# Kernel optimization log

Measured on AMD Instinct MI355X. Metric: run time of the kernel, lower is better.

Reference implementation:

```python
import jax, jax.numpy as jnp
import numpy as np

HEADS = 8
DIM_HEAD = 64
SCALE = DIM_HEAD ** -0.5


def setup_inputs() -> dict:
    key = jax.random.key(0)
    k1, k2, k3, k4 = jax.random.split(key, 4)
    dim = 512
    inner = HEADS * DIM_HEAD  # 512
    x = jax.random.normal(k1, (4, 2048, dim), dtype=jnp.float32)
    # torch nn.Linear weight layout: [out_features, in_features]
    w_qkv = jax.random.normal(k2, (inner * 3, dim), dtype=jnp.float32) * (dim ** -0.5)
    w_out = jax.random.normal(k3, (dim, inner), dtype=jnp.float32) * (inner ** -0.5)
    b_out = jax.random.normal(k4, (dim,), dtype=jnp.float32) * 0.01
    return {"x": x, "w_qkv": w_qkv, "w_out": w_out, "b_out": b_out}


def reference(x, w_qkv, w_out, b_out):
    b, n, _ = x.shape
    qkv = x @ w_qkv.T                                   # [b, n, 3*inner]
    q, k, v = jnp.split(qkv, 3, axis=-1)
    def to_heads(t):
        return t.reshape(b, n, HEADS, DIM_HEAD).transpose(0, 2, 1, 3)  # b h n d
    q, k, v = to_heads(q), to_heads(k), to_heads(v)
    dots = jnp.einsum('bhid,bhjd->bhij', q, k) * SCALE  # [b, h, n, n]
    attn = jax.nn.softmax(dots, axis=-1)
    out = jnp.einsum('bhij,bhjd->bhid', attn, v)        # [b, h, n, d]
    out = out.transpose(0, 2, 1, 3).reshape(b, n, HEADS * DIM_HEAD)
    return out @ w_out.T + b_out                        # [b, n, dim]
```

## Files before the change

kernel.cpp:

```cpp
#include <hip/hip_runtime.h>

typedef unsigned int u32;
typedef unsigned short u16;
typedef float f32x4 __attribute__((ext_vector_type(4)));
typedef u32 u32x4 __attribute__((ext_vector_type(4)));
typedef u32 u32x2 __attribute__((ext_vector_type(2)));

__device__ __forceinline__ u16 f2bf(float f) {
    u32 u = __builtin_bit_cast(u32, f);
    u = (u + 0x7FFFu + ((u >> 16) & 1u)) >> 16;
    return (u16)u;
}

__device__ __forceinline__ void mfma16(f32x4& d, const u32x4& a, const u32x4& b) {
    asm("v_mfma_f32_16x16x32_bf16 %0, %1, %2, %0" : "+v"(d) : "v"(a), "v"(b));
}

__device__ __forceinline__ float exp2a(float x) {
    float r;
    asm("v_exp_f32 %0, %1\n\ts_nop 1" : "=v"(r) : "v"(x));
    return r;
}
__device__ __forceinline__ u32 cvtpk(float lo, float hi) {
    u32 r;
    asm("v_cvt_pk_bf16_f32 %0, %1, %2" : "=v"(r) : "v"(lo), "v"(hi));
    return r;
}
__device__ __forceinline__ void gload_lds16(const u16* g, u16* l) {
    __builtin_amdgcn_global_load_lds(
        (const __attribute__((address_space(1))) u32*)g,
        (__attribute__((address_space(3))) u32*)l, 16, 0, 0);
}

__global__ __launch_bounds__(256) void cast2_kernel(
    const float* __restrict__ wq, const float* __restrict__ wo,
    u16* __restrict__ wqb, u16* __restrict__ wob) {
    int bid = blockIdx.x;
    const float* src;
    u16* dst;
    int base;
    if (bid < 384) { src = wq; dst = wqb; base = bid * 2048; }
    else           { src = wo; dst = wob; base = (bid - 384) * 2048; }
    int i = base + threadIdx.x * 8;
    float4 a = *(const float4*)(src + i);
    float4 b = *(const float4*)(src + i + 4);
    u32x4 r;
    r.x = (u32)f2bf(a.x) | ((u32)f2bf(a.y) << 16);
    r.y = (u32)f2bf(a.z) | ((u32)f2bf(a.w) << 16);
    r.z = (u32)f2bf(b.x) | ((u32)f2bf(b.y) << 16);
    r.w = (u32)f2bf(b.z) | ((u32)f2bf(b.w) << 16);
    *(u32x4*)(dst + i) = r;
}

__global__ __launch_bounds__(256) void gemm_qkv(
    const float* __restrict__ A32, const u16* __restrict__ B, int K,
    u16* __restrict__ qo, u16* __restrict__ ko, u16* __restrict__ vto)
{
    __shared__ __align__(16) u16 Al[128 * 64];
    __shared__ __align__(16) u16 Bl[128 * 64];
    const int t = threadIdx.x;
    const int w = t >> 6, l = t & 63;
    const int wr = w >> 1, wc = w & 1;
    const int g = l >> 4, li = l & 15;
    const int m0 = blockIdx.x * 128, n0 = blockIdx.y * 128;

    const f32x4 z = {0.f, 0.f, 0.f, 0.f};
    f32x4 acc[4][4];
#pragma unroll
    for (int mi = 0; mi < 4; ++mi)
#pragma unroll
        for (int ni = 0; ni < 4; ++ni) acc[mi][ni] = z;

    int goff[4], ldst[4];
#pragma unroll
    for (int rnd = 0; rnd < 4; ++rnd) {
        int s = rnd * 256 + t;
        int p = s >> 3, cp = s & 7;
        int cg = cp ^ (p & 7);
        goff[rnd] = p * K + cg * 8;
        ldst[rnd] = s * 8;
    }

    for (int k0 = 0; k0 < K; k0 += 64) {
        __syncthreads();
#pragma unroll
        for (int rnd = 0; rnd < 4; ++rnd) {
            const float* src = A32 + (size_t)m0 * K + k0 + goff[rnd];
            float4 fa = *(const float4*)src;
            float4 fb = *(const float4*)(src + 4);
            u32x4 vv;
            vv.x = cvtpk(fa.x, fa.y);
            vv.y = cvtpk(fa.z, fa.w);
            vv.z = cvtpk(fb.x, fb.y);
            vv.w = cvtpk(fb.z, fb.w);
            *(u32x4*)&Al[ldst[rnd]] = vv;
        }
#pragma unroll
        for (int rnd = 0; rnd < 4; ++rnd)
            gload_lds16(B + (size_t)n0 * K + k0 + goff[rnd], &Bl[ldst[rnd]]);
        __syncthreads();
#pragma unroll
        for (int ks = 0; ks < 2; ++ks) {
            u32x4 af[4], bf[4];
#pragma unroll
            for (int mi = 0; mi < 4; ++mi)
                af[mi] = *(const u32x4*)&Al[(wr * 64 + mi * 16 + li) * 64
                                            + (((ks * 4 + g) ^ (li & 7)) * 8)];
#pragma unroll
            for (int ni = 0; ni < 4; ++ni)
                bf[ni] = *(const u32x4*)&Bl[(wc * 64 + ni * 16 + li) * 64
                                            + (((ks * 4 + g) ^ (li & 7)) * 8)];
#pragma unroll
            for (int mi = 0; mi < 4; ++mi)
#pragma unroll
                for (int ni = 0; ni < 4; ++ni) mfma16(acc[mi][ni], af[mi], bf[ni]);
        }
    }

#pragma unroll
    for (int mi = 0; mi < 4; ++mi) {
#pragma unroll
        for (int ni = 0; ni < 4; ++ni) {
            int o = n0 + wc * 64 + ni * 16 + li;
            int m_base = m0 + wr * 64 + mi * 16 + g * 4;
            int part = o >> 9, oi = o & 511;
            int h = oi >> 6, d = oi & 63;
            int bb = m_base >> 11, nn = m_base & 2047;
            if (part == 2) {
                u32x2 pv;
                pv.x = (u32)f2bf(acc[mi][ni][0]) | ((u32)f2bf(acc[mi][ni][1]) << 16);
                pv.y = (u32)f2bf(acc[mi][ni][2]) | ((u32)f2bf(acc[mi][ni][3]) << 16);
                *(u32x2*)(vto + ((size_t)(bb * 8 + h) * 64 + d) * 2048 + nn) = pv;
            } else {
                u16* dst = (part == 0) ? qo : ko;
#pragma unroll
                for (int r = 0; r < 4; ++r)
                    dst[((size_t)(bb * 8 + h) * 2048 + nn + r) * 64 + d] =
                        f2bf(acc[mi][ni][r]);
            }
        }
    }
}

__global__ __launch_bounds__(256) void gemm_out(
    const u16* __restrict__ A16, const u16* __restrict__ B,
    float* __restrict__ fo, const float* __restrict__ bias)
{
    const int K = 512, N = 512;
    __shared__ __align__(16) u16 Al[128 * 64];
    __shared__ __align__(16) u16 Bl[64 * 64];
    const int t = threadIdx.x;
    const int w = t >> 6, l = t & 63;
    const int wr = w >> 1, wc = w & 1;
    const int g = l >> 4, li = l & 15;
    const int m0 = blockIdx.x * 128, n0 = blockIdx.y * 64;

    const f32x4 z = {0.f, 0.f, 0.f, 0.f};
    f32x4 acc[4][2];
#pragma unroll
    for (int mi = 0; mi < 4; ++mi)
#pragma unroll
        for (int ni = 0; ni < 2; ++ni) acc[mi][ni] = z;

    int goffA[4], ldstA[4], goffB[2], ldstB[2];
#pragma unroll
    for (int rnd = 0; rnd < 4; ++rnd) {
        int s = rnd * 256 + t;
        int p = s >> 3, cp = s & 7;
        int cg = cp ^ (p & 7);
        goffA[rnd] = p * K + cg * 8;
        ldstA[rnd] = s * 8;
    }
#pragma unroll
    for (int rnd = 0; rnd < 2; ++rnd) {
        int s = rnd * 256 + t;
        int p = s >> 3, cp = s & 7;
        int cg = cp ^ (p & 7);
        goffB[rnd] = p * K + cg * 8;
        ldstB[rnd] = s * 8;
    }

    for (int k0 = 0; k0 < K; k0 += 64) {
        __syncthreads();
#pragma unroll
        for (int rnd = 0; rnd < 4; ++rnd)
            gload_lds16(A16 + (size_t)m0 * K + k0 + goffA[rnd], &Al[ldstA[rnd]]);
#pragma unroll
        for (int rnd = 0; rnd < 2; ++rnd)
            gload_lds16(B + (size_t)n0 * K + k0 + goffB[rnd], &Bl[ldstB[rnd]]);
        __syncthreads();
#pragma unroll
        for (int ks = 0; ks < 2; ++ks) {
            u32x4 af[4], bf[2];
#pragma unroll
            for (int mi = 0; mi < 4; ++mi)
                af[mi] = *(const u32x4*)&Al[(wr * 64 + mi * 16 + li) * 64
                                            + (((ks * 4 + g) ^ (li & 7)) * 8)];
#pragma unroll
            for (int ni = 0; ni < 2; ++ni)
                bf[ni] = *(const u32x4*)&Bl[(wc * 32 + ni * 16 + li) * 64
                                            + (((ks * 4 + g) ^ (li & 7)) * 8)];
#pragma unroll
            for (int mi = 0; mi < 4; ++mi)
#pragma unroll
                for (int ni = 0; ni < 2; ++ni) mfma16(acc[mi][ni], af[mi], bf[ni]);
        }
    }

#pragma unroll
    for (int mi = 0; mi < 4; ++mi) {
#pragma unroll
        for (int ni = 0; ni < 2; ++ni) {
            int o = n0 + wc * 32 + ni * 16 + li;
            int m_base = m0 + wr * 64 + mi * 16 + g * 4;
#pragma unroll
            for (int r = 0; r < 4; ++r)
                fo[(size_t)(m_base + r) * N + o] = acc[mi][ni][r] + bias[o];
        }
    }
}

__global__ __launch_bounds__(256) void attn_kernel(
    const u16* __restrict__ Q, const u16* __restrict__ Kg,
    const u16* __restrict__ VT, u16* __restrict__ O)
{
    __shared__ __align__(16) u16 Kl[64 * 64];
    __shared__ __align__(16) u16 Vl[64 * 64];
    const int t = threadIdx.x;
    const int w = t >> 6, l = t & 63;
    const int g = l >> 4, li = l & 15;
    const int pair = blockIdx.y;
    const int q0 = blockIdx.x * 128 + w * 32;
    const float CEXP = 0.18033688011112042f;

    u32x4 qf[2][2];
#pragma unroll
    for (int qb = 0; qb < 2; ++qb)
#pragma unroll
        for (int f = 0; f < 2; ++f)
            qf[qb][f] = *(const u32x4*)(Q + ((size_t)pair * 2048 + q0 + qb * 16 + li) * 64
                                          + f * 32 + g * 8);

    const f32x4 z = {0.f, 0.f, 0.f, 0.f};
    f32x4 oacc[2][4];
#pragma unroll
    for (int qb = 0; qb < 2; ++qb)
#pragma unroll
        for (int dc = 0; dc < 4; ++dc) oacc[qb][dc] = z;
    float m_r[2] = {-1e30f, -1e30f};
    float l_r[2] = {0.f, 0.f};

    for (int kt = 0; kt < 32; ++kt) {
        __syncthreads();
#pragma unroll
        for (int i = 0; i < 2; ++i) {
            int s = i * 256 + t;
            int p = s >> 3, cp = s & 7;
            int cg = (cp ^ (p & 7)) * 8;
            int kr = (p & 0x23) | ((p & 0x0C) << 1) | ((p & 0x10) >> 2);
            u32x4 kv = *(const u32x4*)(Kg + ((size_t)pair * 2048 + kt * 64 + kr) * 64 + cg);
            u32x4 vv = *(const u32x4*)(VT + ((size_t)pair * 64 + p) * 2048 + kt * 64 + cg);
            *(u32x4*)&Kl[p * 64 + cp * 8] = kv;
            *(u32x4*)&Vl[p * 64 + cp * 8] = vv;
        }
        __syncthreads();

        f32x4 st[2][4];
#pragma unroll
        for (int qb = 0; qb < 2; ++qb)
#pragma unroll
            for (int kc = 0; kc < 4; ++kc) st[qb][kc] = z;
#pragma unroll
        for (int kc = 0; kc < 4; ++kc)
#pragma unroll
            for (int f = 0; f < 2; ++f) {
                u32x4 kf = *(const u32x4*)&Kl[(kc * 16 + li) * 64
                                              + (((4 * f + g) ^ (li & 7)) * 8)];
                mfma16(st[0][kc], kf, qf[0][f]);
                mfma16(st[1][kc], kf, qf[1][f]);
            }

        u32x4 pb[2][2];
#pragma unroll
        for (int qb = 0; qb < 2; ++qb) {
            float a0 = fmaxf(fmaxf(st[qb][0][0], st[qb][0][1]), fmaxf(st[qb][0][2], st[qb][0][3]));
            float a1 = fmaxf(fmaxf(st[qb][1][0], st[qb][1][1]), fmaxf(st[qb][1][2], st[qb][1][3]));
            float a2 = fmaxf(fmaxf(st[qb][2][0], st[qb][2][1]), fmaxf(st[qb][2][2], st[qb][2][3]));
            float a3 = fmaxf(fmaxf(st[qb][3][0], st[qb][3][1]), fmaxf(st[qb][3][2], st[qb][3][3]));
            float tmax = fmaxf(fmaxf(a0, a1), fmaxf(a2, a3)) * CEXP;
            if (__any(tmax - m_r[qb] > 8.0f)) {
                float m4 = tmax;
                m4 = fmaxf(m4, __shfl_xor(m4, 16));
                m4 = fmaxf(m4, __shfl_xor(m4, 32));
                float mn = fmaxf(m_r[qb], m4);
                float alpha = exp2a(m_r[qb] - mn);
                m_r[qb] = mn;
                l_r[qb] *= alpha;
#pragma unroll
                for (int dc = 0; dc < 4; ++dc) oacc[qb][dc] *= alpha;
            }
            float nm = -m_r[qb];
            float ls0 = 0.f, ls1 = 0.f;
#pragma unroll
            for (int kc = 0; kc < 4; ++kc) {
#pragma unroll
                for (int r = 0; r < 4; ++r) {
                    float pv = exp2a(__builtin_fmaf(st[qb][kc][r], CEXP, nm));
                    st[qb][kc][r] = pv;
                    if (r & 1) ls1 += pv; else ls0 += pv;
                }
            }
            l_r[qb] += ls0 + ls1;
#pragma unroll
            for (int f = 0; f < 2; ++f) {
                u32x4 pk;
                pk.x = cvtpk(st[qb][2 * f][0], st[qb][2 * f][1]);
                pk.y = cvtpk(st[qb][2 * f][2], st[qb][2 * f][3]);
                pk.z = cvtpk(st[qb][2 * f + 1][0], st[qb][2 * f + 1][1]);
                pk.w = cvtpk(st[qb][2 * f + 1][2], st[qb][2 * f + 1][3]);
                pb[qb][f] = pk;
            }
        }

#pragma unroll
        for (int dc = 0; dc < 4; ++dc)
#pragma unroll
            for (int f = 0; f < 2; ++f) {
                u32x4 vf = *(const u32x4*)&Vl[(dc * 16 + li) * 64
                                              + (((4 * f + g) ^ (li & 7)) * 8)];
                mfma16(oacc[0][dc], vf, pb[0][f]);
                mfma16(oacc[1][dc], vf, pb[1][f]);
            }
    }

    const int bb = pair >> 3, h = pair & 7;
#pragma unroll
    for (int qb = 0; qb < 2; ++qb) {
        float ls = l_r[qb];
        ls += __shfl_xor(ls, 16);
        ls += __shfl_xor(ls, 32);
        float inv = 1.f / ls;
        u16* orow = O + ((size_t)bb * 2048 + q0 + qb * 16 + li) * 512 + h * 64;
#pragma unroll
        for (int dc = 0; dc < 4; ++dc) {
            u32x2 pv;
            pv.x = cvtpk(oacc[qb][dc][0] * inv, oacc[qb][dc][1] * inv);
            pv.y = cvtpk(oacc[qb][dc][2] * inv, oacc[qb][dc][3] * inv);
            *(u32x2*)(orow + dc * 16 + 4 * g) = pv;
        }
    }
}

extern "C" void kernel_launch(void* const* d_in, const int* in_sizes, int n_in,
                              void* d_out, int out_size, void* d_ws, size_t ws_size,
                              hipStream_t stream) {
    const float* x     = (const float*)d_in[0];
    const float* w_qkv = (const float*)d_in[1];
    const float* w_out = (const float*)d_in[2];
    const float* b_out = (const float*)d_in[3];
    float* out = (float*)d_out;

    char* ws = (char*)d_ws;
    u16* o  = (u16*)(ws + 0);
    u16* wq = (u16*)(ws + 8388608);
    u16* wo = (u16*)(ws + 9961472);
    u16* q  = (u16*)(ws + 10485760);
    u16* kk = (u16*)(ws + 18874368);
    u16* vt = (u16*)(ws + 27262976);

    cast2_kernel<<<512, 256, 0, stream>>>(w_qkv, w_out, wq, wo);

    gemm_qkv<<<dim3(64, 12), 256, 0, stream>>>(x, wq, 512, q, kk, vt);
    attn_kernel<<<dim3(16, 32), 256, 0, stream>>>(q, kk, vt, o);

    gemm_out<<<dim3(64, 8), 256, 0, stream>>>(o, wo, out, b_out);
}
```

Baseline: 98.58 us.

## Split attention over two KV halves and merge partials in a combine kernel

The attention kernel now launches a third grid dimension that splits the 2048 keys into two halves. Each block writes an unnormalized bf16 partial output plus its running row max and sum. A new combine kernel rescales and merges the two partials and writes the final head-interleaved output. This doubles the number of blocks to improve GPU occupancy, at the cost of an extra launch, extra global memory traffic for the partials, and bf16 rounding of the partial results.

```diff
diff --git a/kernel.cpp b/kernel.cpp
--- a/kernel.cpp
+++ b/kernel.cpp
@@ -10,6 +10,9 @@
     u32 u = __builtin_bit_cast(u32, f);
     u = (u + 0x7FFFu + ((u >> 16) & 1u)) >> 16;
     return (u16)u;
+}
+__device__ __forceinline__ float b2f(u32 h) {
+    return __builtin_bit_cast(float, h << 16);
 }
 
 __device__ __forceinline__ void mfma16(f32x4& d, const u32x4& a, const u32x4& b) {
@@ -222,7 +225,8 @@
 
 __global__ __launch_bounds__(256) void attn_kernel(
     const u16* __restrict__ Q, const u16* __restrict__ Kg,
-    const u16* __restrict__ VT, u16* __restrict__ O)
+    const u16* __restrict__ VT, u16* __restrict__ Op,
+    float* __restrict__ Lp, float* __restrict__ Mp)
 {
     __shared__ __align__(16) u16 Kl[64 * 64];
     __shared__ __align__(16) u16 Vl[64 * 64];
@@ -230,6 +234,7 @@
     const int w = t >> 6, l = t & 63;
     const int g = l >> 4, li = l & 15;
     const int pair = blockIdx.y;
+    const int zs = blockIdx.z;
     const int q0 = blockIdx.x * 128 + w * 32;
     const float CEXP = 0.18033688011112042f;
 
@@ -250,7 +255,7 @@
     float m_r[2] = {-1e30f, -1e30f};
     float l_r[2] = {0.f, 0.f};
 
-    for (int kt = 0; kt < 32; ++kt) {
+    for (int kt = zs * 16; kt < zs * 16 + 16; ++kt) {
         __syncthreads();
 #pragma unroll
         for (int i = 0; i < 2; ++i) {
@@ -333,22 +338,53 @@
             }
     }
 
-    const int bb = pair >> 3, h = pair & 7;
 #pragma unroll
     for (int qb = 0; qb < 2; ++qb) {
         float ls = l_r[qb];
         ls += __shfl_xor(ls, 16);
         ls += __shfl_xor(ls, 32);
-        float inv = 1.f / ls;
-        u16* orow = O + ((size_t)bb * 2048 + q0 + qb * 16 + li) * 512 + h * 64;
+        int zrow = (zs * 32 + pair) * 2048 + q0 + qb * 16 + li;
+        u16* porow = Op + (size_t)zrow * 64;
 #pragma unroll
         for (int dc = 0; dc < 4; ++dc) {
             u32x2 pv;
-            pv.x = cvtpk(oacc[qb][dc][0] * inv, oacc[qb][dc][1] * inv);
-            pv.y = cvtpk(oacc[qb][dc][2] * inv, oacc[qb][dc][3] * inv);
-            *(u32x2*)(orow + dc * 16 + 4 * g) = pv;
-        }
-    }
+            pv.x = cvtpk(oacc[qb][dc][0], oacc[qb][dc][1]);
+            pv.y = cvtpk(oacc[qb][dc][2], oacc[qb][dc][3]);
+            *(u32x2*)(porow + dc * 16 + 4 * g) = pv;
+        }
+        if (g == 0) {
+            Lp[zrow] = ls;
+            Mp[zrow] = m_r[qb];
+        }
+    }
+}
+
+__global__ __launch_bounds__(256) void combine_kernel(
+    const u16* __restrict__ Op, const float* __restrict__ Lp,
+    const float* __restrict__ Mp, u16* __restrict__ O)
+{
+    int tg = blockIdx.x * 256 + threadIdx.x;
+    int row = tg >> 3;
+    int dch = (tg & 7) * 8;
+    float m1 = Mp[row], m2 = Mp[65536 + row];
+    float l1 = Lp[row], l2 = Lp[65536 + row];
+    float m = fmaxf(m1, m2);
+    float c1 = __builtin_exp2f(m1 - m), c2 = __builtin_exp2f(m2 - m);
+    float inv = 1.f / __builtin_fmaf(c1, l1, c2 * l2);
+    float s1 = c1 * inv, s2 = c2 * inv;
+    u32x4 a = *(const u32x4*)(Op + (size_t)row * 64 + dch);
+    u32x4 b = *(const u32x4*)(Op + (size_t)(65536 + row) * 64 + dch);
+    u32x4 r;
+#pragma unroll
+    for (int j = 0; j < 4; ++j) {
+        u32 av = a[j], bv = b[j];
+        float lo = b2f(av & 0xFFFFu) * s1 + b2f(bv & 0xFFFFu) * s2;
+        float hi = b2f(av >> 16) * s1 + b2f(bv >> 16) * s2;
+        r[j] = cvtpk(lo, hi);
+    }
+    int pair = row >> 11, n = row & 2047;
+    int bb = pair >> 3, h = pair & 7;
+    *(u32x4*)(O + ((size_t)(bb * 2048 + n) * 512 + h * 64 + dch)) = r;
 }
 
 extern "C" void kernel_launch(void* const* d_in, const int* in_sizes, int n_in,
@@ -361,17 +397,22 @@
     float* out = (float*)d_out;
 
     char* ws = (char*)d_ws;
-    u16* o  = (u16*)(ws + 0);
-    u16* wq = (u16*)(ws + 8388608);
-    u16* wo = (u16*)(ws + 9961472);
-    u16* q  = (u16*)(ws + 10485760);
-    u16* kk = (u16*)(ws + 18874368);
-    u16* vt = (u16*)(ws + 27262976);
+    u16*   o  = (u16*)(ws + 0);
+    u16*   wq = (u16*)(ws + 8388608);
+    u16*   wo = (u16*)(ws + 9961472);
+    u16*   q  = (u16*)(ws + 10485760);
+    u16*   kk = (u16*)(ws + 18874368);
+    u16*   vt = (u16*)(ws + 27262976);
+    u16*   op = (u16*)(ws + 35651584);
+    float* lp = (float*)(ws + 52428800);
+    float* mp = (float*)(ws + 52953088);
 
     cast2_kernel<<<512, 256, 0, stream>>>(w_qkv, w_out, wq, wo);
 
     gemm_qkv<<<dim3(64, 12), 256, 0, stream>>>(x, wq, 512, q, kk, vt);
-    attn_kernel<<<dim3(16, 32), 256, 0, stream>>>(q, kk, vt, o);
+
+    attn_kernel<<<dim3(16, 32, 2), 256, 0, stream>>>(q, kk, vt, op, lp, mp);
+    combine_kernel<<<2048, 256, 0, stream>>>(op, lp, mp, o);
 
     gemm_out<<<dim3(64, 8), 256, 0, stream>>>(o, wo, out, b_out);
 }
```

Result: slower. 103.2 us (+4.7%).
